# Performance work log

Hardware: AMD Instinct MI355X
Metric: run time of the kernel (lower is better)

Reference implementation:

```python
import jax, jax.numpy as jnp
import numpy as np

N = 500_000
B = 10_000
L = N // B  # 50 tokens per session
H = 128


def setup_inputs() -> dict:
    key = jax.random.key(0)
    ks = jax.random.split(key, 7)
    x = jax.random.normal(ks[0], (N, H), dtype=jnp.float32)
    # sorted segment ids: B sessions of length L (every segment non-empty)
    batch = jnp.repeat(jnp.arange(B, dtype=jnp.int32), L)
    # index of the last element of each session
    last_ixs = jnp.arange(B, dtype=jnp.int32) * L + (L - 1)
    s = 1.0 / np.sqrt(H)
    W1_w = jax.random.uniform(ks[1], (H, H), jnp.float32, -s, s)
    W1_b = jax.random.uniform(ks[2], (H,), jnp.float32, -s, s)
    W2_w = jax.random.uniform(ks[3], (H, H), jnp.float32, -s, s)
    W2_b = jax.random.uniform(ks[4], (H,), jnp.float32, -s, s)
    q_w = jax.random.uniform(ks[5], (1, H), jnp.float32, -s, s)
    q_b = jax.random.uniform(ks[6], (1,), jnp.float32, -s, s)
    return {"x": x, "W1_w": W1_w, "W1_b": W1_b, "W2_w": W2_w, "W2_b": W2_b,
            "q_w": q_w, "q_b": q_b, "batch": batch, "last_ixs": last_ixs,
            "num_segments": B}


def reference(x, W1_w, W1_b, W2_w, W2_b, q_w, q_b, batch, last_ixs, num_segments):
    # v_i = x[last_ixs]; repeat_interleave(v_i, bincount(batch)) == v_i[batch] (batch sorted)
    v_n_repeat = x[last_ixs][batch]                                   # [N, H]
    h = jax.nn.sigmoid(v_n_repeat @ W1_w.T + W1_b + x @ W2_w.T + W2_b)  # [N, H]
    e = (h @ q_w.T + q_b)[:, 0]                                       # [N]
    # segment-wise (per-session) numerically-stable softmax
    m = jax.ops.segment_max(e, batch, num_segments=num_segments)      # [B]
    z = jnp.exp(e - m[batch])                                         # [N]
    denom = jax.ops.segment_sum(z, batch, num_segments=num_segments)  # [B]
    alpha = (z / denom[batch])[:, None]                               # [N, 1]
    # scatter_add pooling of alpha * x over sessions
    s_g = jax.ops.segment_sum(alpha * x, batch, num_segments=num_segments)  # [B, H]
    return s_g
```

## Files before the change

kernel.cpp:

```cpp
#include <hip/hip_runtime.h>

#define H_DIM 128
#define L_SESS 50
#define B_SESS 10000
#define NBLK 768
#define NITER 14
#define LDSTR 136
#define ESTR 5

typedef __bf16 bf16_t;
typedef __bf16 bf16x8 __attribute__((ext_vector_type(8)));
typedef float f32x4 __attribute__((ext_vector_type(4)));

__device__ __forceinline__ bf16x8 cvt_bf8(float4 a, float4 b) {
  bf16x8 r;
  r[0] = (bf16_t)a.x; r[1] = (bf16_t)a.y; r[2] = (bf16_t)a.z; r[3] = (bf16_t)a.w;
  r[4] = (bf16_t)b.x; r[5] = (bf16_t)b.y; r[6] = (bf16_t)b.z; r[7] = (bf16_t)b.w;
  return r;
}

__global__ __launch_bounds__(256, 3) void fused_attn_kernel(
    const float* __restrict__ x, const float* __restrict__ w1,
    const float* __restrict__ w1b, const float* __restrict__ w2,
    const float* __restrict__ w2bi, const float* __restrict__ qw,
    const float* __restrict__ qb, float* __restrict__ out) {
  __shared__ __attribute__((aligned(16))) unsigned short Xb[64 * LDSTR];
  __shared__ float epart[64 * ESTR];
  __shared__ float alpha_s[64];

  const int t = threadIdx.x;
  const int lane = t & 63, w = t >> 6, q = lane >> 4, c = lane & 15;
  const int n0 = w * 32 + c, n1 = n0 + 16;

  int s = blockIdx.x;
  int sc = (s < B_SESS) ? s : (B_SESS - 1);
  const float4* xv = (const float4*)(x + (size_t)sc * (L_SESS * H_DIM));
  float4 v[6];
#pragma unroll
  for (int j = 0; j < 6; ++j) v[j] = xv[t + 256 * j];
  float4 v6;
  if (t < 64) v6 = xv[1536 + t];

  bf16x8 bw2[4][2], bw1[4][2];
  const float4* w2v = (const float4*)w2;
  const float4* w1v = (const float4*)w1;
#pragma unroll
  for (int kt = 0; kt < 4; ++kt) {
    const int ko4 = kt * 8 + q * 2;
    bw2[kt][0] = cvt_bf8(w2v[n0 * 32 + ko4], w2v[n0 * 32 + ko4 + 1]);
    bw2[kt][1] = cvt_bf8(w2v[n1 * 32 + ko4], w2v[n1 * 32 + ko4 + 1]);
    bw1[kt][0] = cvt_bf8(w1v[n0 * 32 + ko4], w1v[n0 * 32 + ko4 + 1]);
    bw1[kt][1] = cvt_bf8(w1v[n1 * 32 + ko4], w1v[n1 * 32 + ko4 + 1]);
  }
  const float qn0 = qw[n0], qn1 = qw[n1], qbv = qb[0];
  const float b0 = w1b[n0] + w2bi[n0];
  const float b1 = w1b[n1] + w2bi[n1];

  const f32x4 zero4 = {0.f, 0.f, 0.f, 0.f};

  for (int it = 0; it < NITER; ++it) {
    __syncthreads();

#pragma unroll
    for (int j = 0; j < 6; ++j) {
      int i = t + 256 * j;
      int row = i >> 5, col = (i & 31) * 4;
      union { bf16_t h[4]; ushort4 u4; } tmp;
      tmp.h[0] = (bf16_t)v[j].x; tmp.h[1] = (bf16_t)v[j].y;
      tmp.h[2] = (bf16_t)v[j].z; tmp.h[3] = (bf16_t)v[j].w;
      *(ushort4*)&Xb[row * LDSTR + col] = tmp.u4;
    }
    if (t < 64) {
      int i = 1536 + t;
      int row = i >> 5, col = (i & 31) * 4;
      union { bf16_t h[4]; ushort4 u4; } tmp;
      tmp.h[0] = (bf16_t)v6.x; tmp.h[1] = (bf16_t)v6.y;
      tmp.h[2] = (bf16_t)v6.z; tmp.h[3] = (bf16_t)v6.w;
      *(ushort4*)&Xb[row * LDSTR + col] = tmp.u4;
    }
    __syncthreads();

    if (it + 1 < NITER) {
      int sn = s + NBLK;
      int snc = (sn < B_SESS) ? sn : (B_SESS - 1);
      const float4* xn = (const float4*)(x + (size_t)snc * (L_SESS * H_DIM));
#pragma unroll
      for (int j = 0; j < 6; ++j) v[j] = xn[t + 256 * j];
      if (t < 64) v6 = xn[1536 + t];
    }

    f32x4 uacc0 = zero4, uacc1 = zero4;
#pragma unroll
    for (int kt = 0; kt < 4; ++kt) {
      bf16x8 av = *(const bf16x8*)&Xb[49 * LDSTR + kt * 32 + q * 8];
      uacc0 = __builtin_amdgcn_mfma_f32_16x16x32_bf16(av, bw1[kt][0], uacc0, 0, 0, 0);
      uacc1 = __builtin_amdgcn_mfma_f32_16x16x32_bf16(av, bw1[kt][1], uacc1, 0, 0, 0);
    }
    const float u0 = uacc0[0] + b0;
    const float u1 = uacc1[0] + b1;

    f32x4 acc[4][2];
#pragma unroll
    for (int mt = 0; mt < 4; ++mt) { acc[mt][0] = zero4; acc[mt][1] = zero4; }
#pragma unroll
    for (int kt = 0; kt < 4; ++kt) {
      const int ko = kt * 32 + q * 8;
#pragma unroll
      for (int mt = 0; mt < 4; ++mt) {
        bf16x8 a = *(const bf16x8*)&Xb[(mt * 16 + c) * LDSTR + ko];
        acc[mt][0] = __builtin_amdgcn_mfma_f32_16x16x32_bf16(a, bw2[kt][0], acc[mt][0], 0, 0, 0);
        acc[mt][1] = __builtin_amdgcn_mfma_f32_16x16x32_bf16(a, bw2[kt][1], acc[mt][1], 0, 0, 0);
      }
    }

#pragma unroll
    for (int mt = 0; mt < 4; ++mt) {
#pragma unroll
      for (int r = 0; r < 4; ++r) {
        float t0 = acc[mt][0][r] + u0;
        float t1 = acc[mt][1][r] + u1;
        float h0 = 1.0f / (1.0f + __expf(-t0));
        float h1 = 1.0f / (1.0f + __expf(-t1));
        float p = h0 * qn0 + h1 * qn1;
#pragma unroll
        for (int off = 1; off <= 8; off <<= 1) p += __shfl_xor(p, off);
        if (c == 0) epart[(mt * 16 + q * 4 + r) * ESTR + w] = p;
      }
    }
    __syncthreads();

    if (t < 64) {
      float e = qbv;
#pragma unroll
      for (int j = 0; j < 4; ++j) e += epart[t * ESTR + j];
      float val = (t < L_SESS) ? e : -1.0e30f;
      float mx = val;
#pragma unroll
      for (int off = 32; off > 0; off >>= 1) mx = fmaxf(mx, __shfl_xor(mx, off));
      float z = (t < L_SESS) ? __expf(e - mx) : 0.f;
      float d = z;
#pragma unroll
      for (int off = 32; off > 0; off >>= 1) d += __shfl_xor(d, off);
      alpha_s[t] = z / d;
    }
    __syncthreads();

    if (t < H_DIM) {
      float acc_p = 0.f;
#pragma unroll
      for (int m = 0; m < L_SESS; ++m) {
        unsigned short pv = Xb[m * LDSTR + t];
        acc_p += alpha_s[m] * __uint_as_float(((unsigned int)pv) << 16);
      }
      if (s < B_SESS) out[(size_t)s * H_DIM + t] = acc_p;
    }
    s += NBLK;
  }
}

extern "C" void kernel_launch(void* const* d_in, const int* in_sizes, int n_in,
                              void* d_out, int out_size, void* d_ws, size_t ws_size,
                              hipStream_t stream) {
  const float* x    = (const float*)d_in[0];
  const float* w1   = (const float*)d_in[1];
  const float* w1b  = (const float*)d_in[2];
  const float* w2   = (const float*)d_in[3];
  const float* w2bi = (const float*)d_in[4];
  const float* qw   = (const float*)d_in[5];
  const float* qb   = (const float*)d_in[6];
  fused_attn_kernel<<<NBLK, 256, 0, stream>>>(x, w1, w1b, w2, w2bi, qw, qb,
                                              (float*)d_out);
}
```

Baseline: 387.4 us.

## Use DPP reductions, redundant per-wave softmax, and split pooling across all waves

Replaces the shuffle-based 16-lane sums with DPP row reductions, and uses a select so each lane does a single epart store per wave. Every wave now computes the segment softmax redundantly instead of only wave 0, which drops one block barrier. The alpha-weighted pooling is split across all four waves, each handling a quarter of the rows with readlane broadcasts of alpha and two columns per lane, then partials are combined through a small LDS buffer. It aims to cut serial pooling latency and barrier count, at the cost of extra LDS traffic and duplicated softmax work.

After: 378.3 us. -2.3%, faster.

```diff
diff --git a/kernel.cpp b/kernel.cpp
--- a/kernel.cpp
+++ b/kernel.cpp
@@ -7,6 +7,7 @@
 #define NITER 14
 #define LDSTR 136
 #define ESTR 5
+#define POOLSTR 132
 
 typedef __bf16 bf16_t;
 typedef __bf16 bf16x8 __attribute__((ext_vector_type(8)));
@@ -17,6 +18,35 @@
   r[0] = (bf16_t)a.x; r[1] = (bf16_t)a.y; r[2] = (bf16_t)a.z; r[3] = (bf16_t)a.w;
   r[4] = (bf16_t)b.x; r[5] = (bf16_t)b.y; r[6] = (bf16_t)b.z; r[7] = (bf16_t)b.w;
   return r;
+}
+
+template <int CTRL>
+__device__ __forceinline__ float dpp_add(float x) {
+  int tt = __builtin_amdgcn_update_dpp(0, __float_as_int(x), CTRL, 0xF, 0xF, false);
+  return x + __int_as_float(tt);
+}
+template <int CTRL>
+__device__ __forceinline__ float dpp_max(float x) {
+  int tt = __builtin_amdgcn_update_dpp(0, __float_as_int(x), CTRL, 0xF, 0xF, false);
+  return fmaxf(x, __int_as_float(tt));
+}
+__device__ __forceinline__ float row16_sum(float x) {
+  x = dpp_add<0x121>(x); x = dpp_add<0x122>(x);
+  x = dpp_add<0x124>(x); x = dpp_add<0x128>(x);
+  return x;
+}
+__device__ __forceinline__ float wave_sum(float x) {
+  x = row16_sum(x);
+  x += __shfl_xor(x, 16);
+  x += __shfl_xor(x, 32);
+  return x;
+}
+__device__ __forceinline__ float wave_max(float x) {
+  x = dpp_max<0x121>(x); x = dpp_max<0x122>(x);
+  x = dpp_max<0x124>(x); x = dpp_max<0x128>(x);
+  x = fmaxf(x, __shfl_xor(x, 16));
+  x = fmaxf(x, __shfl_xor(x, 32));
+  return x;
 }
 
 __global__ __launch_bounds__(256, 3) void fused_attn_kernel(
@@ -25,11 +55,12 @@
     const float* __restrict__ w2bi, const float* __restrict__ qw,
     const float* __restrict__ qb, float* __restrict__ out) {
   __shared__ __attribute__((aligned(16))) unsigned short Xb[64 * LDSTR];
-  __shared__ float epart[64 * ESTR];
-  __shared__ float alpha_s[64];
+  __shared__ __attribute__((aligned(16))) float epart[64 * ESTR];
+  __shared__ __attribute__((aligned(16))) float pool[4 * POOLSTR];
 
   const int t = threadIdx.x;
   const int lane = t & 63, w = t >> 6, q = lane >> 4, c = lane & 15;
+  const int wu = __builtin_amdgcn_readfirstlane(w);
   const int n0 = w * 32 + c, n1 = n0 + 16;
 
   int s = blockIdx.x;
@@ -113,6 +144,7 @@
       }
     }
 
+    float esel = 0.f;
 #pragma unroll
     for (int mt = 0; mt < 4; ++mt) {
 #pragma unroll
@@ -122,37 +154,41 @@
         float h0 = 1.0f / (1.0f + __expf(-t0));
         float h1 = 1.0f / (1.0f + __expf(-t1));
         float p = h0 * qn0 + h1 * qn1;
-#pragma unroll
-        for (int off = 1; off <= 8; off <<= 1) p += __shfl_xor(p, off);
-        if (c == 0) epart[(mt * 16 + q * 4 + r) * ESTR + w] = p;
+        p = row16_sum(p);
+        esel = (c == mt * 4 + r) ? p : esel;
       }
     }
-    __syncthreads();
-
-    if (t < 64) {
-      float e = qbv;
-#pragma unroll
-      for (int j = 0; j < 4; ++j) e += epart[t * ESTR + j];
-      float val = (t < L_SESS) ? e : -1.0e30f;
-      float mx = val;
-#pragma unroll
-      for (int off = 32; off > 0; off >>= 1) mx = fmaxf(mx, __shfl_xor(mx, off));
-      float z = (t < L_SESS) ? __expf(e - mx) : 0.f;
-      float d = z;
-#pragma unroll
-      for (int off = 32; off > 0; off >>= 1) d += __shfl_xor(d, off);
-      alpha_s[t] = z / d;
-    }
+    epart[((c >> 2) * 16 + q * 4 + (c & 3)) * ESTR + wu] = esel;
+    __syncthreads();
+
+    float e = qbv;
+#pragma unroll
+    for (int j = 0; j < 4; ++j) e += epart[lane * ESTR + j];
+    float mval = (lane < L_SESS) ? e : -1.0e30f;
+    float mx = wave_max(mval);
+    float z = (lane < L_SESS) ? __expf(e - mx) : 0.f;
+    float d = wave_sum(z);
+    float alpha = z / d;
+
+    float p0 = 0.f, p1 = 0.f;
+#pragma unroll
+    for (int k = 0; k < 13; ++k) {
+      int m = wu + 4 * k;
+      if (m < L_SESS) {
+        float am = __int_as_float(
+            __builtin_amdgcn_readlane(__float_as_int(alpha), m));
+        unsigned int xv2 = *(const unsigned int*)&Xb[m * LDSTR + 2 * lane];
+        p0 += am * __uint_as_float(xv2 << 16);
+        p1 += am * __uint_as_float(xv2 & 0xFFFF0000u);
+      }
+    }
+    *(float2*)&pool[wu * POOLSTR + 2 * lane] = make_float2(p0, p1);
     __syncthreads();
 
     if (t < H_DIM) {
-      float acc_p = 0.f;
-#pragma unroll
-      for (int m = 0; m < L_SESS; ++m) {
-        unsigned short pv = Xb[m * LDSTR + t];
-        acc_p += alpha_s[m] * __uint_as_float(((unsigned int)pv) << 16);
-      }
-      if (s < B_SESS) out[(size_t)s * H_DIM + t] = acc_p;
+      float r = pool[t] + pool[POOLSTR + t] + pool[2 * POOLSTR + t] +
+                pool[3 * POOLSTR + t];
+      if (s < B_SESS) out[(size_t)s * H_DIM + t] = r;
     }
     s += NBLK;
   }
```
